# Performance work log

Measured on AMD Instinct MI355X. Metric: run time of the kernel, lower is better.

Reference implementation:

```python
import jax, jax.numpy as jnp
import numpy as np
from jax import lax

SEQ_LEN = 131072
EMBED_DIM = 256
DT = 0.1
EPS = 1e-8


def setup_inputs() -> dict:
    key = jax.random.key(0)
    k1, k2, k3, k4 = jax.random.split(key, 4)
    psi_real = jax.random.normal(k1, (SEQ_LEN, EMBED_DIM), dtype=jnp.float32)
    psi_imag = jax.random.normal(k2, (SEQ_LEN, EMBED_DIM), dtype=jnp.float32)
    # Hermitian Hamiltonian: H = (A + A^H)/2 with A ~ 0.1*randn (complex)
    a_re = jax.random.normal(k3, (EMBED_DIM, EMBED_DIM), dtype=jnp.float32) * 0.1
    a_im = jax.random.normal(k4, (EMBED_DIM, EMBED_DIM), dtype=jnp.float32) * 0.1
    ham_real = (a_re + a_re.T) / 2.0   # symmetric real part
    ham_imag = (a_im - a_im.T) / 2.0   # antisymmetric imag part
    hbar = jnp.ones((1,), dtype=jnp.float32)
    return {"psi_real": psi_real, "psi_imag": psi_imag,
            "ham_real": ham_real, "ham_imag": ham_imag,
            "hbar": hbar, "time_steps": 10}


def reference(psi_real, psi_imag, ham_real, ham_imag, hbar, time_steps):
    psi = psi_real + 1j * psi_imag                      # [S, D] complex64
    H = ham_real + 1j * ham_imag                        # [D, D] complex64
    coef = (-1j / hbar[0].astype(jnp.complex64)) * DT   # scalar complex

    def step(p, _):
        h_psi = p @ H.T                                 # [S, D] complex matmul
        p = p + coef * h_psi                            # Schrodinger Euler step
        norms = jnp.sqrt(jnp.sum(p.real * p.real + p.imag * p.imag,
                                 axis=1, keepdims=True))  # torch.norm over dim=1
        return p / (norms + EPS), None

    psi_out, _ = lax.scan(step, psi, None, length=time_steps)
    return psi_out
```

## Files before the change

### kernel.cpp

```cpp
#include <hip/hip_runtime.h>

#define SEQ 131072
#define DIM 256
#define DTC 0.1f
#define EPSC 1e-8f

typedef __attribute__((ext_vector_type(8))) short bf16x8;
typedef __attribute__((ext_vector_type(4))) float f32x4;
typedef __attribute__((ext_vector_type(4))) int   i32x4;

static __device__ __forceinline__ unsigned short f2bf(float f){
  unsigned int u = __builtin_bit_cast(unsigned int, f);
  u += 0x7fffu + ((u >> 16) & 1u);
  return (unsigned short)(u >> 16);
}

__global__ __launch_bounds__(256)
void k_first(const float* __restrict__ hr, const float* __restrict__ hi,
             const float* __restrict__ hbar, const int* __restrict__ ts,
             float* __restrict__ m1r, float* __restrict__ m1i,
             float* __restrict__ ar,  float* __restrict__ ai)
{
  const int idx = blockIdx.x * 256 + threadIdx.x;
  const int r = idx >> 8, c = idx & 255;
  const float s = DTC / hbar[0];
  const float diag = (r == c) ? 1.0f : 0.0f;
  const float mr = diag + s * hi[idx];
  const float mi =       -s * hr[idx];
  m1r[idx] = mr;  m1i[idx] = mi;
  const bool b = ((ts[0] >> 4) & 1) != 0;
  ar[idx] = b ? mr : diag;
  ai[idx] = b ? mi : 0.0f;
}

template<int BIT>
__global__ __launch_bounds__(1024)
void k_step2(const float* __restrict__ inr, const float* __restrict__ ini,
             const float* __restrict__ m1r, const float* __restrict__ m1i,
             const int* __restrict__ ts,
             float* __restrict__ outr, float* __restrict__ outi)
{
  __shared__ float rr[256], ri[256];
  __shared__ float pr_[4][256], pi_[4][256];
  const int tid = threadIdx.x, c = tid & 255, q = tid >> 8;
  const int r = blockIdx.x;
  if (q == 0){ rr[c] = inr[r*256 + c]; ri[c] = ini[r*256 + c]; }
  __syncthreads();

  float ar = 0.f, ai = 0.f;
  const int k0 = q * 64;
  #pragma unroll 8
  for (int k = k0; k < k0 + 64; ++k){
    const float br = inr[k*256 + c], bi = ini[k*256 + c];
    const float xr = rr[k],          xi = ri[k];
    ar = fmaf(xr, br, fmaf(-xi, bi, ar));
    ai = fmaf(xr, bi, fmaf( xi, br, ai));
  }
  pr_[q][c] = ar; pi_[q][c] = ai;
  __syncthreads();

  const bool bit = ((ts[0] >> BIT) & 1) != 0;
  if (!bit){
    if (q == 0){
      outr[r*256+c] = pr_[0][c]+pr_[1][c]+pr_[2][c]+pr_[3][c];
      outi[r*256+c] = pi_[0][c]+pi_[1][c]+pi_[2][c]+pi_[3][c];
    }
    return;
  }
  if (q == 0){
    rr[c] = pr_[0][c]+pr_[1][c]+pr_[2][c]+pr_[3][c];
    ri[c] = pi_[0][c]+pi_[1][c]+pi_[2][c]+pi_[3][c];
  }
  __syncthreads();
  ar = 0.f; ai = 0.f;
  #pragma unroll 8
  for (int k = k0; k < k0 + 64; ++k){
    const float br = m1r[k*256 + c], bi = m1i[k*256 + c];
    const float xr = rr[k],          xi = ri[k];
    ar = fmaf(xr, br, fmaf(-xi, bi, ar));
    ai = fmaf(xr, bi, fmaf( xi, br, ai));
  }
  pr_[q][c] = ar; pi_[q][c] = ai;
  __syncthreads();
  if (q == 0){
    outr[r*256+c] = pr_[0][c]+pr_[1][c]+pr_[2][c]+pr_[3][c];
    outi[r*256+c] = pi_[0][c]+pi_[1][c]+pi_[2][c]+pi_[3][c];
  }
}

__global__ __launch_bounds__(1024)
void k_last2(const float* __restrict__ inr, const float* __restrict__ ini,
             const float* __restrict__ m1r, const float* __restrict__ m1i,
             const int* __restrict__ ts,
             float* __restrict__ outr, float* __restrict__ outi,
             unsigned short* __restrict__ fragbuf)
{
  __shared__ float rr[256], ri[256];
  __shared__ float pr_[4][256], pi_[4][256];
  const int tid = threadIdx.x, c = tid & 255, q = tid >> 8;
  const int r = blockIdx.x;
  if (q == 0){ rr[c] = inr[r*256 + c]; ri[c] = ini[r*256 + c]; }
  __syncthreads();

  float ar = 0.f, ai = 0.f;
  const int k0 = q * 64;
  #pragma unroll 8
  for (int k = k0; k < k0 + 64; ++k){
    const float br = inr[k*256 + c], bi = ini[k*256 + c];
    const float xr = rr[k],          xi = ri[k];
    ar = fmaf(xr, br, fmaf(-xi, bi, ar));
    ai = fmaf(xr, bi, fmaf( xi, br, ai));
  }
  pr_[q][c] = ar; pi_[q][c] = ai;
  __syncthreads();

  const bool bit = (ts[0] & 1) != 0;
  if (bit){
    if (q == 0){
      rr[c] = pr_[0][c]+pr_[1][c]+pr_[2][c]+pr_[3][c];
      ri[c] = pi_[0][c]+pi_[1][c]+pi_[2][c]+pi_[3][c];
    }
    __syncthreads();
    ar = 0.f; ai = 0.f;
    #pragma unroll 8
    for (int k = k0; k < k0 + 64; ++k){
      const float br = m1r[k*256 + c], bi = m1i[k*256 + c];
      const float xr = rr[k],          xi = ri[k];
      ar = fmaf(xr, br, fmaf(-xi, bi, ar));
      ai = fmaf(xr, bi, fmaf( xi, br, ai));
    }
    pr_[q][c] = ar; pi_[q][c] = ai;
    __syncthreads();
  }

  if (q == 0){
    const float orr = pr_[0][c]+pr_[1][c]+pr_[2][c]+pr_[3][c];
    const float oii = pi_[0][c]+pi_[1][c]+pi_[2][c]+pi_[3][c];
    outr[r*256+c] = orr;
    outi[r*256+c] = oii;
    if (fragbuf){
      const int C = r, K = c;
      const int ftid = (C>>5)*64 + ((K>>3)&3)*16 + (C&15);
      const int fid  = (((C>>4)&1)*8 + (K>>5))*2;
      fragbuf[((size_t)fid*512     + ftid)*8 + (K&7)] = f2bf(orr - ((r==c)?1.0f:0.0f));
      fragbuf[((size_t)(fid+1)*512 + ftid)*8 + (K&7)] = f2bf(oii);
    }
  }
}

template<int STORE_COMPLEX>
__global__ __launch_bounds__(512, 4)
void apply4(const float* __restrict__ psi_re, const float* __restrict__ psi_im,
            const unsigned short* __restrict__ fragbuf,
            const int* __restrict__ tsteps, float* __restrict__ out)
{
  __shared__ alignas(16) unsigned short a_re[32][272];
  __shared__ alignas(16) unsigned short a_im[32][272];
  __shared__ float partials[32][8];

  const int tid  = threadIdx.x;
  const int wv   = tid >> 6;
  const int lane = tid & 63;
  const int lq   = lane >> 4;
  const int lr   = lane & 15;
  const int brow = blockIdx.x << 5;
  const int cbase = wv << 5;
  const int T = tsteps[0];
  const bf16x8* fb = reinterpret_cast<const bf16x8*>(fragbuf);

  float sre[2][2][4], simg[2][2][4];
  #pragma unroll
  for (int rt = 0; rt < 2; ++rt)
    #pragma unroll
    for (int ct = 0; ct < 2; ++ct)
      #pragma unroll
      for (int j = 0; j < 4; ++j){
        const int row = brow + rt*16 + lq*4 + j;
        const int col = cbase + ct*16 + lr;
        const float xr = psi_re[(size_t)row*DIM + col];
        const float xi = psi_im[(size_t)row*DIM + col];
        sre [rt][ct][j] = xr;
        simg[rt][ct][j] = xi;
        a_re[rt*16 + lq*4 + j][col] = f2bf(xr);
        a_im[rt*16 + lq*4 + j][col] = f2bf(xi);
      }
  __syncthreads();

  f32x4 ar[2][2], ai[2][2];
  #pragma unroll
  for (int rt = 0; rt < 2; ++rt)
    #pragma unroll
    for (int ct = 0; ct < 2; ++ct){
      ar[rt][ct] = (f32x4){0.f,0.f,0.f,0.f};
      ai[rt][ct] = (f32x4){0.f,0.f,0.f,0.f};
    }

  #pragma unroll
  for (int kt = 0; kt < 8; ++kt){
    const bf16x8 br0 = fb[((0*8 + kt)*2 + 0)*512 + tid];
    const bf16x8 bi0 = fb[((0*8 + kt)*2 + 1)*512 + tid];
    const bf16x8 br1 = fb[((1*8 + kt)*2 + 0)*512 + tid];
    const bf16x8 bi1 = fb[((1*8 + kt)*2 + 1)*512 + tid];
    #pragma unroll
    for (int rt = 0; rt < 2; ++rt){
      const bf16x8 apr = *reinterpret_cast<const bf16x8*>(&a_re[rt*16 + lr][kt*32 + lq*8]);
      const bf16x8 api = *reinterpret_cast<const bf16x8*>(&a_im[rt*16 + lr][kt*32 + lq*8]);
      const i32x4 tneg = __builtin_bit_cast(i32x4, api) ^ (i32x4)(int)0x80008000;
      const bf16x8 apin = __builtin_bit_cast(bf16x8, tneg);
      ar[rt][0] = __builtin_amdgcn_mfma_f32_16x16x32_bf16(apr,  br0, ar[rt][0], 0,0,0);
      ar[rt][0] = __builtin_amdgcn_mfma_f32_16x16x32_bf16(apin, bi0, ar[rt][0], 0,0,0);
      ai[rt][0] = __builtin_amdgcn_mfma_f32_16x16x32_bf16(apr,  bi0, ai[rt][0], 0,0,0);
      ai[rt][0] = __builtin_amdgcn_mfma_f32_16x16x32_bf16(api,  br0, ai[rt][0], 0,0,0);
      ar[rt][1] = __builtin_amdgcn_mfma_f32_16x16x32_bf16(apr,  br1, ar[rt][1], 0,0,0);
      ar[rt][1] = __builtin_amdgcn_mfma_f32_16x16x32_bf16(apin, bi1, ar[rt][1], 0,0,0);
      ai[rt][1] = __builtin_amdgcn_mfma_f32_16x16x32_bf16(apr,  bi1, ai[rt][1], 0,0,0);
      ai[rt][1] = __builtin_amdgcn_mfma_f32_16x16x32_bf16(api,  br1, ai[rt][1], 0,0,0);
    }
  }

  #pragma unroll
  for (int rt = 0; rt < 2; ++rt)
    #pragma unroll
    for (int j = 0; j < 4; ++j){
      sre [rt][0][j] += ar[rt][0][j];
      simg[rt][0][j] += ai[rt][0][j];
      sre [rt][1][j] += ar[rt][1][j];
      simg[rt][1][j] += ai[rt][1][j];
      float v = sre[rt][0][j]*sre[rt][0][j] + simg[rt][0][j]*simg[rt][0][j]
              + sre[rt][1][j]*sre[rt][1][j] + simg[rt][1][j]*simg[rt][1][j];
      v += __shfl_xor(v, 1);
      v += __shfl_xor(v, 2);
      v += __shfl_xor(v, 4);
      v += __shfl_xor(v, 8);
      if (lr == 0) partials[rt*16 + lq*4 + j][wv] = v;
    }
  __syncthreads();

  #pragma unroll
  for (int rt = 0; rt < 2; ++rt)
    #pragma unroll
    for (int j = 0; j < 4; ++j){
      const int rl = rt*16 + lq*4 + j;
      const f32x4 p0 = *reinterpret_cast<const f32x4*>(&partials[rl][0]);
      const f32x4 p1 = *reinterpret_cast<const f32x4*>(&partials[rl][4]);
      const float nrm = ((p0[0]+p0[1]) + (p0[2]+p0[3]))
                      + ((p1[0]+p1[1]) + (p1[2]+p1[3]));
      const float sc = (T == 0) ? 1.0f : 1.0f/(sqrtf(nrm) + EPSC);
      const size_t off = (size_t)(brow + rl)*DIM + cbase + lr;
      if (STORE_COMPLEX){
        float2 v0 = {sre[rt][0][j]*sc, simg[rt][0][j]*sc};
        float2 v1 = {sre[rt][1][j]*sc, simg[rt][1][j]*sc};
        *reinterpret_cast<float2*>(&out[off*2])      = v0;
        *reinterpret_cast<float2*>(&out[(off+16)*2]) = v1;
      } else {
        out[off]    = sre[rt][0][j]*sc;
        out[off+16] = sre[rt][1][j]*sc;
      }
    }
}

template<int STORE_COMPLEX>
__global__ __launch_bounds__(512, 2)
void apply_kernel(const float* __restrict__ psi_re, const float* __restrict__ psi_im,
                  const float* __restrict__ Pre,    const float* __restrict__ Pim,
                  const int* __restrict__ tsteps,   float* __restrict__ out)
{
  __shared__ alignas(16) unsigned short a_re[64][272];
  __shared__ alignas(16) unsigned short a_im[64][272];
  __shared__ float partials[64][8];
  __shared__ float scales[64];

  const int tid  = threadIdx.x;
  const int wv   = tid >> 6;
  const int lane = tid & 63;
  const int lq   = lane >> 4;
  const int lr   = lane & 15;
  const int brow = blockIdx.x << 6;
  const int cbase = wv << 5;
  const int T = tsteps[0];

  bf16x8 bhr[2][8], bhi[2][8];
  #pragma unroll
  for (int ct = 0; ct < 2; ++ct){
    const int c = cbase + ct*16 + lr;
    #pragma unroll
    for (int kt = 0; kt < 8; ++kt){
      const int kb = kt*32 + lq*8;
      const float4 pr0 = *reinterpret_cast<const float4*>(&Pre[c*DIM + kb]);
      const float4 pr1 = *reinterpret_cast<const float4*>(&Pre[c*DIM + kb + 4]);
      const float4 pi0 = *reinterpret_cast<const float4*>(&Pim[c*DIM + kb]);
      const float4 pi1 = *reinterpret_cast<const float4*>(&Pim[c*DIM + kb + 4]);
      const float re8[8] = {pr0.x,pr0.y,pr0.z,pr0.w, pr1.x,pr1.y,pr1.z,pr1.w};
      const float im8[8] = {pi0.x,pi0.y,pi0.z,pi0.w, pi1.x,pi1.y,pi1.z,pi1.w};
      bf16x8 vr, vi;
      #pragma unroll
      for (int i = 0; i < 8; ++i){
        const float rv = re8[i] - ((c == kb + i) ? 1.0f : 0.0f);
        vr[i] = (short)f2bf(rv);
        vi[i] = (short)f2bf(im8[i]);
      }
      bhr[ct][kt] = vr; bhi[ct][kt] = vi;
    }
  }

  float sre[4][2][4], simg[4][2][4];
  #pragma unroll
  for (int rt = 0; rt < 4; ++rt)
    #pragma unroll
    for (int ct = 0; ct < 2; ++ct)
      #pragma unroll
      for (int j = 0; j < 4; ++j){
        const int row = brow + rt*16 + lq*4 + j;
        const int col = cbase + ct*16 + lr;
        const float xr = psi_re[row*DIM + col];
        const float xi = psi_im[row*DIM + col];
        sre [rt][ct][j] = xr;
        simg[rt][ct][j] = xi;
        a_re[rt*16 + lq*4 + j][col] = f2bf(xr);
        a_im[rt*16 + lq*4 + j][col] = f2bf(xi);
      }
  __syncthreads();

  #pragma unroll
  for (int rt = 0; rt < 4; ++rt){
    f32x4 ar0 = {0.f,0.f,0.f,0.f}, ar1 = {0.f,0.f,0.f,0.f};
    f32x4 ai0 = {0.f,0.f,0.f,0.f}, ai1 = {0.f,0.f,0.f,0.f};
    #pragma unroll
    for (int kt = 0; kt < 8; ++kt){
      const int arow = rt*16 + lr;
      const int kofs = kt*32 + lq*8;
      bf16x8 apr = *reinterpret_cast<const bf16x8*>(&a_re[arow][kofs]);
      bf16x8 api = *reinterpret_cast<const bf16x8*>(&a_im[arow][kofs]);
      i32x4 tneg = __builtin_bit_cast(i32x4, api) ^ (i32x4)(int)0x80008000;
      bf16x8 apin = __builtin_bit_cast(bf16x8, tneg);
      ar0 = __builtin_amdgcn_mfma_f32_16x16x32_bf16(apr,  bhr[0][kt], ar0, 0,0,0);
      ai0 = __builtin_amdgcn_mfma_f32_16x16x32_bf16(apr,  bhi[0][kt], ai0, 0,0,0);
      ar1 = __builtin_amdgcn_mfma_f32_16x16x32_bf16(apr,  bhr[1][kt], ar1, 0,0,0);
      ai1 = __builtin_amdgcn_mfma_f32_16x16x32_bf16(apr,  bhi[1][kt], ai1, 0,0,0);
      ar0 = __builtin_amdgcn_mfma_f32_16x16x32_bf16(apin, bhi[0][kt], ar0, 0,0,0);
      ai0 = __builtin_amdgcn_mfma_f32_16x16x32_bf16(api,  bhr[0][kt], ai0, 0,0,0);
      ar1 = __builtin_amdgcn_mfma_f32_16x16x32_bf16(apin, bhi[1][kt], ar1, 0,0,0);
      ai1 = __builtin_amdgcn_mfma_f32_16x16x32_bf16(api,  bhr[1][kt], ai1, 0,0,0);
    }
    float ss[4];
    #pragma unroll
    for (int j = 0; j < 4; ++j){
      sre [rt][0][j] += ar0[j];
      simg[rt][0][j] += ai0[j];
      sre [rt][1][j] += ar1[j];
      simg[rt][1][j] += ai1[j];
      float v = sre[rt][0][j]*sre[rt][0][j] + simg[rt][0][j]*simg[rt][0][j]
              + sre[rt][1][j]*sre[rt][1][j] + simg[rt][1][j]*simg[rt][1][j];
      v += __shfl_xor(v, 1);
      v += __shfl_xor(v, 2);
      v += __shfl_xor(v, 4);
      v += __shfl_xor(v, 8);
      ss[j] = v;
    }
    if (lr == 0){
      #pragma unroll
      for (int j = 0; j < 4; ++j)
        partials[rt*16 + lq*4 + j][wv] = ss[j];
    }
  }
  __syncthreads();

  if (tid < 64){
    float acc = 0.f;
    #pragma unroll
    for (int w = 0; w < 8; ++w) acc += partials[tid][w];
    scales[tid] = (T == 0) ? 1.0f : 1.0f / (sqrtf(acc) + EPSC);
  }
  __syncthreads();

  #pragma unroll
  for (int rt = 0; rt < 4; ++rt)
    #pragma unroll
    for (int ct = 0; ct < 2; ++ct)
      #pragma unroll
      for (int j = 0; j < 4; ++j){
        const int row = brow + rt*16 + lq*4 + j;
        const int col = cbase + ct*16 + lr;
        const float sc = scales[rt*16 + lq*4 + j];
        const float xr = sre [rt][ct][j] * sc;
        const float xi = simg[rt][ct][j] * sc;
        if (STORE_COMPLEX){
          float2 v2 = {xr, xi};
          *reinterpret_cast<float2*>(&out[(size_t)(row*DIM + col)*2]) = v2;
        } else {
          out[row*DIM + col] = xr;
        }
      }
}

template<int STORE_COMPLEX>
__global__ __launch_bounds__(512, 2)
void qevolve_kernel(const float* __restrict__ psi_re, const float* __restrict__ psi_im,
                    const float* __restrict__ ham_re, const float* __restrict__ ham_im,
                    const float* __restrict__ hbar,   const int* __restrict__ tsteps,
                    float* __restrict__ out)
{
  __shared__ alignas(16) unsigned short a_re[64][272];
  __shared__ alignas(16) unsigned short a_im[64][272];
  __shared__ float partials[64][8];
  __shared__ float scales[64];

  const int tid  = threadIdx.x;
  const int wv   = tid >> 6;
  const int lane = tid & 63;
  const int lq   = lane >> 4;
  const int lr   = lane & 15;
  const int brow = blockIdx.x << 6;
  const int cbase = wv << 5;
  const float cs = DTC / hbar[0];
  const int T = tsteps[0];

  bf16x8 bhr[2][8], bhi[2][8];
  #pragma unroll
  for (int ct = 0; ct < 2; ++ct){
    const int c = cbase + ct*16 + lr;
    #pragma unroll
    for (int kt = 0; kt < 8; ++kt){
      const int kb = kt*32 + lq*8;
      bf16x8 vr, vi;
      #pragma unroll
      for (int i = 0; i < 8; ++i){
        vr[i] = (short)f2bf(ham_re[c*DIM + kb + i]);
        vi[i] = (short)f2bf(ham_im[c*DIM + kb + i]);
      }
      bhr[ct][kt] = vr; bhi[ct][kt] = vi;
    }
  }

  float sre[4][2][4], simg[4][2][4];
  #pragma unroll
  for (int rt = 0; rt < 4; ++rt)
    #pragma unroll
    for (int ct = 0; ct < 2; ++ct)
      #pragma unroll
      for (int j = 0; j < 4; ++j){
        const int row = brow + rt*16 + lq*4 + j;
        const int col = cbase + ct*16 + lr;
        sre [rt][ct][j] = psi_re[row*DIM + col];
        simg[rt][ct][j] = psi_im[row*DIM + col];
      }

  for (int s = 0; s < T; ++s){
    #pragma unroll
    for (int rt = 0; rt < 4; ++rt)
      #pragma unroll
      for (int ct = 0; ct < 2; ++ct)
        #pragma unroll
        for (int j = 0; j < 4; ++j){
          const int row = rt*16 + lq*4 + j;
          const int col = cbase + ct*16 + lr;
          a_re[row][col] = f2bf(sre [rt][ct][j]);
          a_im[row][col] = f2bf(simg[rt][ct][j]);
        }
    __syncthreads();

    #pragma unroll
    for (int rt = 0; rt < 4; ++rt){
      f32x4 ar0 = {0.f,0.f,0.f,0.f}, ar1 = {0.f,0.f,0.f,0.f};
      f32x4 ai0 = {0.f,0.f,0.f,0.f}, ai1 = {0.f,0.f,0.f,0.f};
      #pragma unroll
      for (int kt = 0; kt < 8; ++kt){
        const int arow = rt*16 + lr;
        const int kofs = kt*32 + lq*8;
        bf16x8 apr = *reinterpret_cast<const bf16x8*>(&a_re[arow][kofs]);
        bf16x8 api = *reinterpret_cast<const bf16x8*>(&a_im[arow][kofs]);
        i32x4 tneg = __builtin_bit_cast(i32x4, api) ^ (i32x4)(int)0x80008000;
        bf16x8 apin = __builtin_bit_cast(bf16x8, tneg);
        ar0 = __builtin_amdgcn_mfma_f32_16x16x32_bf16(apr,  bhr[0][kt], ar0, 0,0,0);
        ai0 = __builtin_amdgcn_mfma_f32_16x16x32_bf16(apr,  bhi[0][kt], ai0, 0,0,0);
        ar1 = __builtin_amdgcn_mfma_f32_16x16x32_bf16(apr,  bhr[1][kt], ar1, 0,0,0);
        ai1 = __builtin_amdgcn_mfma_f32_16x16x32_bf16(apr,  bhi[1][kt], ai1, 0,0,0);
        ar0 = __builtin_amdgcn_mfma_f32_16x16x32_bf16(apin, bhi[0][kt], ar0, 0,0,0);
        ai0 = __builtin_amdgcn_mfma_f32_16x16x32_bf16(api,  bhr[0][kt], ai0, 0,0,0);
        ar1 = __builtin_amdgcn_mfma_f32_16x16x32_bf16(apin, bhi[1][kt], ar1, 0,0,0);
        ai1 = __builtin_amdgcn_mfma_f32_16x16x32_bf16(api,  bhr[1][kt], ai1, 0,0,0);
      }
      float ss[4];
      #pragma unroll
      for (int j = 0; j < 4; ++j){
        sre [rt][0][j] += cs * ai0[j];
        simg[rt][0][j] -= cs * ar0[j];
        sre [rt][1][j] += cs * ai1[j];
        simg[rt][1][j] -= cs * ar1[j];
        float v = sre[rt][0][j]*sre[rt][0][j] + simg[rt][0][j]*simg[rt][0][j]
                + sre[rt][1][j]*sre[rt][1][j] + simg[rt][1][j]*simg[rt][1][j];
        v += __shfl_xor(v, 1);
        v += __shfl_xor(v, 2);
        v += __shfl_xor(v, 4);
        v += __shfl_xor(v, 8);
        ss[j] = v;
      }
      if (lr == 0){
        #pragma unroll
        for (int j = 0; j < 4; ++j)
          partials[rt*16 + lq*4 + j][wv] = ss[j];
      }
    }
    __syncthreads();

    if (tid < 64){
      float acc = 0.f;
      #pragma unroll
      for (int w = 0; w < 8; ++w) acc += partials[tid][w];
      scales[tid] = 1.0f / (sqrtf(acc) + EPSC);
    }
    __syncthreads();

    #pragma unroll
    for (int rt = 0; rt < 4; ++rt)
      #pragma unroll
      for (int j = 0; j < 4; ++j){
        const float sc = scales[rt*16 + lq*4 + j];
        sre [rt][0][j] *= sc; sre [rt][1][j] *= sc;
        simg[rt][0][j] *= sc; simg[rt][1][j] *= sc;
      }
  }

  #pragma unroll
  for (int rt = 0; rt < 4; ++rt)
    #pragma unroll
    for (int ct = 0; ct < 2; ++ct)
      #pragma unroll
      for (int j = 0; j < 4; ++j){
        const int row = brow + rt*16 + lq*4 + j;
        const int col = cbase + ct*16 + lr;
        if (STORE_COMPLEX){
          out[(size_t)(row*DIM + col)*2 + 0] = sre [rt][ct][j];
          out[(size_t)(row*DIM + col)*2 + 1] = simg[rt][ct][j];
        } else {
          out[row*DIM + col] = sre[rt][ct][j];
        }
      }
}

extern "C" void kernel_launch(void* const* d_in, const int* in_sizes, int n_in,
                              void* d_out, int out_size, void* d_ws, size_t ws_size,
                              hipStream_t stream)
{
  const float* psi_re = (const float*)d_in[0];
  const float* psi_im = (const float*)d_in[1];
  const float* ham_re = (const float*)d_in[2];
  const float* ham_im = (const float*)d_in[3];
  const float* hbar   = (const float*)d_in[4];
  const int*   tstep  = (const int*)d_in[5];
  float* out = (float*)d_out;

  const size_t NMAT    = (size_t)DIM * DIM;
  const size_t WS_MAT  = 6 * NMAT * sizeof(float);
  const size_t WS_FRAG = 2 * 8 * 2 * 512 * 16;

  const bool cplx = (out_size == 2 * SEQ * DIM);

  if (d_ws != nullptr && ws_size >= WS_MAT){
    float* w   = (float*)d_ws;
    float* m1r = w + 0*NMAT; float* m1i = w + 1*NMAT;
    float* Ar  = w + 2*NMAT; float* Ai  = w + 3*NMAT;
    float* Br  = w + 4*NMAT; float* Bi  = w + 5*NMAT;
    const bool have_frag = (ws_size >= WS_MAT + WS_FRAG);
    unsigned short* fragbuf = have_frag ? (unsigned short*)(w + 6*NMAT) : nullptr;

    k_first   <<<256, 256,  0, stream>>>(ham_re, ham_im, hbar, tstep, m1r, m1i, Ar, Ai);
    k_step2<3><<<256, 1024, 0, stream>>>(Ar, Ai, m1r, m1i, tstep, Br, Bi);
    k_step2<2><<<256, 1024, 0, stream>>>(Br, Bi, m1r, m1i, tstep, Ar, Ai);
    k_step2<1><<<256, 1024, 0, stream>>>(Ar, Ai, m1r, m1i, tstep, Br, Bi);
    k_last2   <<<256, 1024, 0, stream>>>(Br, Bi, m1r, m1i, tstep, Ar, Ai, fragbuf);

    if (have_frag){
      dim3 grid(SEQ / 32), block(512);
      if (cplx)
        apply4<1><<<grid, block, 0, stream>>>(psi_re, psi_im, fragbuf, tstep, out);
      else
        apply4<0><<<grid, block, 0, stream>>>(psi_re, psi_im, fragbuf, tstep, out);
    } else {
      dim3 grid(SEQ / 64), block(512);
      if (cplx)
        apply_kernel<1><<<grid, block, 0, stream>>>(psi_re, psi_im, Ar, Ai, tstep, out);
      else
        apply_kernel<0><<<grid, block, 0, stream>>>(psi_re, psi_im, Ar, Ai, tstep, out);
    }
  } else {
    dim3 grid(SEQ / 64), block(512);
    if (cplx)
      qevolve_kernel<1><<<grid, block, 0, stream>>>(psi_re, psi_im, ham_re, ham_im, hbar, tstep, out);
    else
      qevolve_kernel<0><<<grid, block, 0, stream>>>(psi_re, psi_im, ham_re, ham_im, hbar, tstep, out);
  }

  (void)in_sizes; (void)n_in;
}
```

Baseline: 242.6 us.

## Fuse matrix-power chain into one cooperative kernel with grid syncs

Replaces the five separate launches that build the propagator matrix (M^T via repeated squaring) with a single cooperative kernel that uses grid.sync between squaring and multiply stages and writes the bf16 fragment buffer directly. The aim is to remove per-launch overhead and the gaps between the small 256x256 matmul kernels. It also hoists the first k-tile of B-fragment loads in the apply kernel ahead of the LDS staging, to overlap that global load with the conversion. The cooperative path depends on the runtime accepting the launch, and falls back to the old kernels otherwise. The matmul inside the cooperative kernel is scalar FMA rather than a tuned one.

```diff
diff --git a/kernel.cpp b/kernel.cpp
--- a/kernel.cpp
+++ b/kernel.cpp
@@ -1,4 +1,7 @@
 #include <hip/hip_runtime.h>
+#include <hip/hip_cooperative_groups.h>
+
+namespace cg = cooperative_groups;
 
 #define SEQ 131072
 #define DIM 256
@@ -13,6 +16,86 @@
   unsigned int u = __builtin_bit_cast(unsigned int, f);
   u += 0x7fffu + ((u >> 16) & 1u);
   return (unsigned short)(u >> 16);
+}
+
+__global__ __launch_bounds__(1024)
+void coop_chain(const float* __restrict__ hr, const float* __restrict__ hi,
+                const float* __restrict__ hbar, const int* __restrict__ ts,
+                float* __restrict__ m1r, float* __restrict__ m1i,
+                float* __restrict__ Ar,  float* __restrict__ Ai,
+                float* __restrict__ Br,  float* __restrict__ Bi,
+                unsigned short* __restrict__ fragbuf)
+{
+  cg::grid_group grid = cg::this_grid();
+  __shared__ float rowr[256], rowi[256];
+  __shared__ float pr_[4][256], pi_[4][256];
+  const int tid = threadIdx.x, c = tid & 255, q = tid >> 8;
+  const int r = blockIdx.x;
+  const float s = DTC / hbar[0];
+  const int T = ts[0];
+
+  if (q == 0){
+    const int idx = r*256 + c;
+    const float diag = (r == c) ? 1.0f : 0.0f;
+    m1r[idx] = diag + s * hi[idx];
+    m1i[idx] =       -s * hr[idx];
+  }
+  grid.sync();
+
+  auto matmul = [&](const float* lr_, const float* li_,
+                    const float* rr_, const float* ri_,
+                    float* or_, float* oi_){
+    if (q == 0){ rowr[c] = lr_[r*256 + c]; rowi[c] = li_[r*256 + c]; }
+    __syncthreads();
+    float ar = 0.f, ai = 0.f;
+    const int k0 = q * 64;
+    #pragma unroll 8
+    for (int k = k0; k < k0 + 64; ++k){
+      const float br = rr_[k*256 + c], bi = ri_[k*256 + c];
+      const float xr = rowr[k],        xi = rowi[k];
+      ar = fmaf(xr, br, fmaf(-xi, bi, ar));
+      ai = fmaf(xr, bi, fmaf( xi, br, ai));
+    }
+    pr_[q][c] = ar; pi_[q][c] = ai;
+    __syncthreads();
+    if (q == 0){
+      or_[r*256+c] = pr_[0][c]+pr_[1][c]+pr_[2][c]+pr_[3][c];
+      oi_[r*256+c] = pi_[0][c]+pi_[1][c]+pi_[2][c]+pi_[3][c];
+    }
+  };
+
+  const float* xr = m1r; const float* xi = m1i;
+  float* dstR[2] = {Ar, Br}; float* dstI[2] = {Ai, Bi};
+  int freeb = 0;
+
+  if (T >= 2){
+    const int msb = 31 - __clz(T);
+    for (int b = msb - 1; b >= 0; --b){
+      matmul(xr, xi, xr, xi, dstR[freeb], dstI[freeb]);
+      grid.sync();
+      xr = dstR[freeb]; xi = dstI[freeb]; freeb ^= 1;
+      if ((T >> b) & 1){
+        matmul(xr, xi, m1r, m1i, dstR[freeb], dstI[freeb]);
+        grid.sync();
+        xr = dstR[freeb]; xi = dstI[freeb]; freeb ^= 1;
+      }
+    }
+  }
+
+  const int idx = r * 1024 + tid;
+  if (idx < 65536){
+    const int C = idx >> 8, K = idx & 255;
+    float vr, vi;
+    if (T == 0){ vr = 0.f; vi = 0.f; }
+    else {
+      vr = xr[C*256 + K] - ((C == K) ? 1.0f : 0.0f);
+      vi = xi[C*256 + K];
+    }
+    const int ftid = (C>>5)*64 + ((K>>3)&3)*16 + (C&15);
+    const int fid  = (((C>>4)&1)*8 + (K>>5))*2;
+    fragbuf[((size_t)fid*512     + ftid)*8 + (K&7)] = f2bf(vr);
+    fragbuf[((size_t)(fid+1)*512 + ftid)*8 + (K&7)] = f2bf(vi);
+  }
 }
 
 __global__ __launch_bounds__(256)
@@ -177,12 +260,23 @@
       for (int j = 0; j < 4; ++j){
         const int row = brow + rt*16 + lq*4 + j;
         const int col = cbase + ct*16 + lr;
-        const float xr = psi_re[(size_t)row*DIM + col];
-        const float xi = psi_im[(size_t)row*DIM + col];
-        sre [rt][ct][j] = xr;
-        simg[rt][ct][j] = xi;
-        a_re[rt*16 + lq*4 + j][col] = f2bf(xr);
-        a_im[rt*16 + lq*4 + j][col] = f2bf(xi);
+        sre [rt][ct][j] = psi_re[(size_t)row*DIM + col];
+        simg[rt][ct][j] = psi_im[(size_t)row*DIM + col];
+      }
+
+  const bf16x8 hb_r0 = fb[( 0)*512 + tid];
+  const bf16x8 hb_i0 = fb[( 1)*512 + tid];
+  const bf16x8 hb_r1 = fb[(16)*512 + tid];
+  const bf16x8 hb_i1 = fb[(17)*512 + tid];
+
+  #pragma unroll
+  for (int rt = 0; rt < 2; ++rt)
+    #pragma unroll
+    for (int ct = 0; ct < 2; ++ct)
+      #pragma unroll
+      for (int j = 0; j < 4; ++j){
+        a_re[rt*16 + lq*4 + j][cbase + ct*16 + lr] = f2bf(sre [rt][ct][j]);
+        a_im[rt*16 + lq*4 + j][cbase + ct*16 + lr] = f2bf(simg[rt][ct][j]);
       }
   __syncthreads();
 
@@ -197,10 +291,14 @@
 
   #pragma unroll
   for (int kt = 0; kt < 8; ++kt){
-    const bf16x8 br0 = fb[((0*8 + kt)*2 + 0)*512 + tid];
-    const bf16x8 bi0 = fb[((0*8 + kt)*2 + 1)*512 + tid];
-    const bf16x8 br1 = fb[((1*8 + kt)*2 + 0)*512 + tid];
-    const bf16x8 bi1 = fb[((1*8 + kt)*2 + 1)*512 + tid];
+    bf16x8 br0, bi0, br1, bi1;
+    if (kt == 0){ br0 = hb_r0; bi0 = hb_i0; br1 = hb_r1; bi1 = hb_i1; }
+    else {
+      br0 = fb[((0*8 + kt)*2 + 0)*512 + tid];
+      bi0 = fb[((0*8 + kt)*2 + 1)*512 + tid];
+      br1 = fb[((1*8 + kt)*2 + 0)*512 + tid];
+      bi1 = fb[((1*8 + kt)*2 + 1)*512 + tid];
+    }
     #pragma unroll
     for (int rt = 0; rt < 2; ++rt){
       const bf16x8 apr = *reinterpret_cast<const bf16x8*>(&a_re[rt*16 + lr][kt*32 + lq*8]);
@@ -564,11 +662,26 @@
     const bool have_frag = (ws_size >= WS_MAT + WS_FRAG);
     unsigned short* fragbuf = have_frag ? (unsigned short*)(w + 6*NMAT) : nullptr;
 
-    k_first   <<<256, 256,  0, stream>>>(ham_re, ham_im, hbar, tstep, m1r, m1i, Ar, Ai);
-    k_step2<3><<<256, 1024, 0, stream>>>(Ar, Ai, m1r, m1i, tstep, Br, Bi);
-    k_step2<2><<<256, 1024, 0, stream>>>(Br, Bi, m1r, m1i, tstep, Ar, Ai);
-    k_step2<1><<<256, 1024, 0, stream>>>(Ar, Ai, m1r, m1i, tstep, Br, Bi);
-    k_last2   <<<256, 1024, 0, stream>>>(Br, Bi, m1r, m1i, tstep, Ar, Ai, fragbuf);
+    bool coop_ok = false;
+    if (have_frag){
+      const float* c0 = ham_re; const float* c1 = ham_im; const float* c2 = hbar;
+      const int* c3 = tstep;
+      float* c4 = m1r; float* c5 = m1i; float* c6 = Ar; float* c7 = Ai;
+      float* c8 = Br;  float* c9 = Bi;  unsigned short* c10 = fragbuf;
+      void* cargs[11] = {&c0,&c1,&c2,&c3,&c4,&c5,&c6,&c7,&c8,&c9,&c10};
+      hipError_t ce = hipLaunchCooperativeKernel(
+          reinterpret_cast<void*>(coop_chain), dim3(256), dim3(1024),
+          cargs, 0, stream);
+      coop_ok = (ce == hipSuccess);
+    }
+
+    if (!coop_ok){
+      k_first   <<<256, 256,  0, stream>>>(ham_re, ham_im, hbar, tstep, m1r, m1i, Ar, Ai);
+      k_step2<3><<<256, 1024, 0, stream>>>(Ar, Ai, m1r, m1i, tstep, Br, Bi);
+      k_step2<2><<<256, 1024, 0, stream>>>(Br, Bi, m1r, m1i, tstep, Ar, Ai);
+      k_step2<1><<<256, 1024, 0, stream>>>(Ar, Ai, m1r, m1i, tstep, Br, Bi);
+      k_last2   <<<256, 1024, 0, stream>>>(Br, Bi, m1r, m1i, tstep, Ar, Ai, fragbuf);
+    }
 
     if (have_frag){
       dim3 grid(SEQ / 32), block(512);
```

New measurement: 340.8 us. +40.5%, slower.
